# Optimization experiments

Measured on AMD Instinct MI355X. Metric: run time of the kernel, lower is better.

The kernel has to match this reference:

```python
import jax, jax.numpy as jnp
import numpy as np

DIM = 192
D_STATE = 16
D_CONV = 4
EXPAND = 2
D_INNER = EXPAND * DIM
DT_RANK = -(-DIM // 16)  # ceil(dim/16) = 12


def setup_inputs() -> dict:
    key = jax.random.key(0)
    ks = jax.random.split(key, 9)
    B, T, H, W, C = 2, 16, 28, 28, DIM
    x = jax.random.normal(ks[0], (B, T, H, W, C), dtype=jnp.float32)
    s = lambda k, shp, fan: jax.random.normal(k, shp, dtype=jnp.float32) / np.sqrt(fan)
    params = {
        "norm_w": jnp.ones((DIM,), jnp.float32),
        "in_proj_w": s(ks[1], (DIM, 2 * D_INNER), DIM),
        "conv_w": s(ks[2], (D_INNER, D_CONV), D_CONV),
        "conv_b": jnp.zeros((D_INNER,), jnp.float32),
        "x_proj_w": s(ks[3], (D_INNER, DT_RANK + 2 * D_STATE), D_INNER),
        "dt_proj_w": s(ks[4], (DT_RANK, D_INNER), DT_RANK),
        "dt_proj_b": jnp.full((D_INNER,), float(np.log(np.expm1(0.01))), jnp.float32),
        "A_log": jnp.log(jnp.broadcast_to(jnp.arange(1, D_STATE + 1, dtype=jnp.float32), (D_INNER, D_STATE))),
        "D": jnp.ones((D_INNER,), jnp.float32),
        "out_proj_w": s(ks[5], (D_INNER, DIM), D_INNER),
    }
    return {"x": x, **params}


def _mamba_block(xs, norm_w, in_proj_w, conv_w, conv_b, x_proj_w,
                 dt_proj_w, dt_proj_b, A_log, D, out_proj_w):
    # xs: (N, T, C). Pre-RMSNorm + Mamba + residual.
    nrm = jax.lax.rsqrt(jnp.mean(xs * xs, axis=-1, keepdims=True) + 1e-6)
    xn = xs * nrm * norm_w

    xz = xn @ in_proj_w                      # (N, T, 2*Din)
    u, z = jnp.split(xz, 2, axis=-1)         # each (N, T, Din)

    # causal depthwise conv over T
    uc = jnp.transpose(u, (0, 2, 1))         # (N, Din, T)
    uc = jax.lax.conv_general_dilated(
        uc, conv_w[:, None, :], window_strides=(1,),
        padding=[(D_CONV - 1, 0)], feature_group_count=D_INNER)
    uc = jax.nn.silu(uc + conv_b[None, :, None])
    uc = jnp.transpose(uc, (0, 2, 1))        # (N, T, Din)

    dbl = uc @ x_proj_w                      # (N, T, dt_rank + 2*S)
    dt, Bm, Cm = jnp.split(dbl, [DT_RANK, DT_RANK + D_STATE], axis=-1)
    dt = jax.nn.softplus(dt @ dt_proj_w + dt_proj_b)   # (N, T, Din)
    A = -jnp.exp(A_log)                      # (Din, S)

    def step(h, inp):
        dt_t, B_t, C_t, u_t = inp            # (N,Din),(N,S),(N,S),(N,Din)
        dA = jnp.exp(dt_t[..., None] * A)    # (N, Din, S)
        h = h * dA + (dt_t * u_t)[..., None] * B_t[:, None, :]
        y = jnp.einsum('nds,ns->nd', h, C_t)
        return h, y

    N = uc.shape[0]
    h0 = jnp.zeros((N, D_INNER, D_STATE), dt.dtype)
    sw = lambda a: jnp.swapaxes(a, 0, 1)     # time-major for scan
    _, ys = jax.lax.scan(step, h0, (sw(dt), sw(Bm), sw(Cm), sw(uc)))
    y = jnp.swapaxes(ys, 0, 1) + uc * D      # (N, T, Din)
    y = y * jax.nn.silu(z)
    return xs + y @ out_proj_w


def reference(x, norm_w, in_proj_w, conv_w, conv_b, x_proj_w,
              dt_proj_w, dt_proj_b, A_log, D, out_proj_w):
    B, T, H, W, C = x.shape
    xs = jnp.transpose(x, (0, 2, 3, 1, 4)).reshape(B * H * W, T, C)
    out = _mamba_block(xs, norm_w, in_proj_w, conv_w, conv_b, x_proj_w,
                       dt_proj_w, dt_proj_b, A_log, D, out_proj_w)
    return jnp.transpose(out.reshape(B, H, W, T, C), (0, 3, 1, 2, 4))
```

## Files before the change

kernel.cpp:

```cpp
#include <hip/hip_runtime.h>

#define NSEQ 1568
#define TDIM 16
#define CDIM 192
#define DIN  384
#define SDIM 16
#define RNK  12
#define XZW  768
#define DBLW 44
#define HW784 784

#define XNP  200
#define DINP 392
#define DBLP 48

#define NT_IN 48
#define KT_IN 6
#define NT_OUT 12
#define KT_OUT 12
#define NT_XP 3
#define KT_XP 12
#define GRP_IN  (NT_IN*KT_IN*64)
#define GRP_OUT (NT_OUT*KT_OUT*64)
#define GRP_XP  (NT_XP*KT_XP*64)
#define OFF_OUT (GRP_IN*8)
#define OFF_XP  (OFF_OUT + GRP_OUT*8)
#define WS_NEED ((size_t)(OFF_XP + GRP_XP*8) * 2)

typedef unsigned short u16;
typedef unsigned int   u32;
typedef __attribute__((ext_vector_type(8))) short short8;
typedef __attribute__((ext_vector_type(4))) float f32x4;

#define LOG2E 1.44269504f
#define LN2   0.69314718f

__device__ __forceinline__ float bf2f(u16 u) {
  union { u32 i; float f; } c; c.i = ((u32)u) << 16; return c.f;
}
__device__ __forceinline__ float asf(u32 i) {
  union { u32 i; float f; } c; c.i = i; return c.f;
}
__device__ __forceinline__ u16 f2bf(float f) {
  union { float f; u32 i; } c; c.f = f;
  u32 i = c.i;
  i += 0x7FFFu + ((i >> 16) & 1u);
  return (u16)(i >> 16);
}

__device__ __forceinline__ float ex2(float x) {
#if __has_builtin(__builtin_amdgcn_exp2f)
  return __builtin_amdgcn_exp2f(x);
#else
  return exp2f(x);
#endif
}
__device__ __forceinline__ float lg2(float x) {
#if __has_builtin(__builtin_amdgcn_logf)
  return __builtin_amdgcn_logf(x);
#else
  return log2f(x);
#endif
}
__device__ __forceinline__ float frcp(float x) {
#if __has_builtin(__builtin_amdgcn_rcpf)
  return __builtin_amdgcn_rcpf(x);
#else
  return 1.0f / x;
#endif
}
__device__ __forceinline__ float sigmoid_f(float s) {
  return frcp(1.0f + ex2(-LOG2E * s));
}
__device__ __forceinline__ float softplus_f(float a) {
  return fmaxf(a, 0.f) + LN2 * lg2(1.0f + ex2(-LOG2E * fabsf(a)));
}

template<bool B16>
__device__ __forceinline__ float ldg(const void* p, int i) {
  if (B16) return bf2f(((const u16*)p)[i]);
  return ((const float*)p)[i];
}
template<bool B16>
__device__ __forceinline__ void stg(void* p, int i, float v) {
  if (B16) ((u16*)p)[i] = f2bf(v);
  else     ((float*)p)[i] = v;
}

__device__ __forceinline__ bool probe_bf16(const void* x) {
  const u16* xu = (const u16*)x;
  int plaus = 0;
  #pragma unroll
  for (int k = 0; k < 32; ++k) {
    u16 v = xu[2*k];
    int e = (v >> 7) & 0xFF;
    plaus += ((e >= 100 && e <= 140) || v == 0) ? 1 : 0;
  }
  return plaus >= 16;
}

template<bool B16>
__device__ __forceinline__ void pack_body(const void* in_w, const void* out_w,
                                          const void* xp_w, u16* ws, int g) {
  if (g < GRP_IN) {
    int lane = g & 63, kt = (g >> 6) % KT_IN, nt = g / (64*KT_IN);
    int k0 = kt*32 + (lane >> 4)*8, n = nt*16 + (lane & 15);
    u16* dst = ws + g*8;
    #pragma unroll
    for (int j = 0; j < 8; ++j) dst[j] = f2bf(ldg<B16>(in_w, (k0+j)*XZW + n));
  } else if (g < GRP_IN + GRP_OUT) {
    int gg = g - GRP_IN;
    int lane = gg & 63, kt = (gg >> 6) % KT_OUT, nt = gg / (64*KT_OUT);
    int k0 = kt*32 + (lane >> 4)*8, n = nt*16 + (lane & 15);
    u16* dst = ws + OFF_OUT + gg*8;
    #pragma unroll
    for (int j = 0; j < 8; ++j) dst[j] = f2bf(ldg<B16>(out_w, (k0+j)*CDIM + n));
  } else if (g < GRP_IN + GRP_OUT + GRP_XP) {
    int gg = g - GRP_IN - GRP_OUT;
    int lane = gg & 63, kt = (gg >> 6) % KT_XP, nt = gg / (64*KT_XP);
    int k0 = kt*32 + (lane >> 4)*8, n = nt*16 + (lane & 15);
    u16* dst = ws + OFF_XP + gg*8;
    #pragma unroll
    for (int j = 0; j < 8; ++j)
      dst[j] = f2bf(n < DBLW ? ldg<B16>(xp_w, (k0+j)*DBLW + n) : 0.f);
  }
}

__global__ void pack_w(const void* __restrict__ x, const void* __restrict__ in_w,
                       const void* __restrict__ out_w, const void* __restrict__ xp_w,
                       u16* __restrict__ ws) {
  int g = blockIdx.x * blockDim.x + threadIdx.x;
  if (probe_bf16(x)) pack_body<true >(in_w, out_w, xp_w, ws, g);
  else               pack_body<false>(in_w, out_w, xp_w, ws, g);
}

struct Smem {
  u16   xn [TDIM*XNP];
  u16   u  [TDIM*DINP];
  u16   z  [TDIM*DINP];
  float dbl[TDIM*DBLP];
};

template<bool B16>
__device__ __forceinline__ void body(
    Smem& sm, const u16* __restrict__ ws,
    const void* __restrict__ x,        const void* __restrict__ norm_w,
    const void* __restrict__ conv_w,   const void* __restrict__ conv_b,
    const void* __restrict__ dt_proj_w,const void* __restrict__ dt_proj_b,
    const void* __restrict__ A_log,    const void* __restrict__ Dp,
    void* __restrict__ out)
{
  const int tid  = threadIdx.x;
  const int wid  = tid >> 6;
  const int lane = tid & 63;
  const int quad = lane >> 4;
  const int l16  = lane & 15;
  const int n  = blockIdx.x;
  const int b  = n / HW784;
  const int hw = n - b * HW784;

  {
    const int c0 = lane, c1 = lane + 64, c2 = lane + 128;
    float nw0 = ldg<B16>(norm_w, c0), nw1 = ldg<B16>(norm_w, c1), nw2 = ldg<B16>(norm_w, c2);
    for (int t = wid; t < TDIM; t += 6) {
      int base = ((b*TDIM + t)*HW784 + hw)*CDIM;
      float v0 = ldg<B16>(x, base + c0);
      float v1 = ldg<B16>(x, base + c1);
      float v2 = ldg<B16>(x, base + c2);
      float ss = v0*v0 + v1*v1 + v2*v2;
      #pragma unroll
      for (int off = 32; off > 0; off >>= 1) ss += __shfl_xor(ss, off, 64);
      float rs = rsqrtf(ss * (1.0f/CDIM) + 1e-6f);
      sm.xn[t*XNP + c0] = f2bf(v0 * rs * nw0);
      sm.xn[t*XNP + c1] = f2bf(v1 * rs * nw1);
      sm.xn[t*XNP + c2] = f2bf(v2 * rs * nw2);
    }
  }
  __syncthreads();

  {
    short8 afr[KT_IN];
    #pragma unroll
    for (int kt = 0; kt < KT_IN; ++kt)
      afr[kt] = *(const short8*)(sm.xn + l16*XNP + kt*32 + quad*8);
    #pragma unroll
    for (int g = 0; g < 2; ++g) {
      f32x4 acc[4];
      #pragma unroll
      for (int i = 0; i < 4; ++i) acc[i] = (f32x4)0.f;
      #pragma unroll
      for (int kt = 0; kt < KT_IN; ++kt) {
        #pragma unroll
        for (int i = 0; i < 4; ++i) {
          int ntg = wid*8 + g*4 + i;
          short8 bfr = *(const short8*)(ws + ((ntg*KT_IN + kt)*64 + lane)*8);
          acc[i] = __builtin_amdgcn_mfma_f32_16x16x32_bf16(afr[kt], bfr, acc[i], 0, 0, 0);
        }
      }
      #pragma unroll
      for (int i = 0; i < 4; ++i) {
        int ntg = wid*8 + g*4 + i;
        u16* dst = (ntg < 24) ? sm.u : sm.z;
        int col = ((ntg < 24) ? ntg*16 : (ntg-24)*16) + l16;
        #pragma unroll
        for (int r = 0; r < 4; ++r)
          dst[(quad*4 + r)*DINP + col] = f2bf(acc[i][r]);
      }
    }
  }
  __syncthreads();

  {
    const int d = tid;
    float uv[TDIM];
    #pragma unroll
    for (int t = 0; t < TDIM; ++t) uv[t] = bf2f(sm.u[t*DINP + d]);
    float w0 = ldg<B16>(conv_w, d*4+0), w1 = ldg<B16>(conv_w, d*4+1);
    float w2 = ldg<B16>(conv_w, d*4+2), w3 = ldg<B16>(conv_w, d*4+3);
    float bias = ldg<B16>(conv_b, d);
    #pragma unroll
    for (int t = 0; t < TDIM; ++t) {
      float s = bias + uv[t]*w3;
      if (t >= 1) s += uv[t-1]*w2;
      if (t >= 2) s += uv[t-2]*w1;
      if (t >= 3) s += uv[t-3]*w0;
      sm.u[t*DINP + d] = f2bf(s * sigmoid_f(s));
    }
  }

  float wd[RNK], A2[SDIM];
  float dt_bias = ldg<B16>(dt_proj_b, tid);
  #pragma unroll
  for (int r = 0; r < RNK; ++r) wd[r] = ldg<B16>(dt_proj_w, r*DIN + tid);
  #pragma unroll
  for (int s = 0; s < SDIM; ++s)
    A2[s] = -LOG2E * ex2(LOG2E * ldg<B16>(A_log, tid*SDIM + s));
  float Dv = ldg<B16>(Dp, tid);
  __syncthreads();

  if (wid < 3) {
    f32x4 acc = (f32x4)0.f;
    #pragma unroll
    for (int kt = 0; kt < KT_XP; ++kt) {
      short8 afr = *(const short8*)(sm.u + l16*DINP + kt*32 + quad*8);
      short8 bfr = *(const short8*)(ws + OFF_XP + ((wid*KT_XP + kt)*64 + lane)*8);
      acc = __builtin_amdgcn_mfma_f32_16x16x32_bf16(afr, bfr, acc, 0, 0, 0);
    }
    #pragma unroll
    for (int r = 0; r < 4; ++r)
      sm.dbl[(quad*4 + r)*DBLP + wid*16 + l16] = acc[r];
  }
  __syncthreads();

  {
    const int d = tid;
    float h[SDIM];
    #pragma unroll
    for (int s = 0; s < SDIM; ++s) h[s] = 0.f;
    for (int t = 0; t < TDIM; ++t) {
      float a = dt_bias;
      #pragma unroll
      for (int r = 0; r < RNK; ++r) a += sm.dbl[t*DBLP + r] * wd[r];
      float dtv = softplus_f(a);
      float uv  = bf2f(sm.u[t*DINP + d]);
      float du  = dtv * uv;
      float y = 0.f;
      #pragma unroll
      for (int s = 0; s < SDIM; ++s) {
        float dA = ex2(dtv * A2[s]);
        h[s] = h[s]*dA + du * sm.dbl[t*DBLP + 12 + s];
        y += h[s] * sm.dbl[t*DBLP + 28 + s];
      }
      y += uv * Dv;
      float zv = bf2f(sm.z[t*DINP + d]);
      sm.z[t*DINP + d] = f2bf(y * (zv * sigmoid_f(zv)));
    }
  }
  __syncthreads();

  {
    f32x4 acc[2];
    acc[0] = (f32x4)0.f; acc[1] = (f32x4)0.f;
    #pragma unroll
    for (int kt = 0; kt < KT_OUT; ++kt) {
      short8 afr = *(const short8*)(sm.z + l16*DINP + kt*32 + quad*8);
      #pragma unroll
      for (int i = 0; i < 2; ++i) {
        int ntg = wid*2 + i;
        short8 bfr = *(const short8*)(ws + OFF_OUT + ((ntg*KT_OUT + kt)*64 + lane)*8);
        acc[i] = __builtin_amdgcn_mfma_f32_16x16x32_bf16(afr, bfr, acc[i], 0, 0, 0);
      }
    }
    #pragma unroll
    for (int i = 0; i < 2; ++i) {
      int col = (wid*2 + i)*16 + l16;
      #pragma unroll
      for (int r = 0; r < 4; ++r) {
        int row = quad*4 + r;
        int gi = ((b*TDIM + row)*HW784 + hw)*CDIM + col;
        float o = ldg<B16>(x, gi) + acc[i][r];
        stg<B16>(out, gi, o);
      }
    }
  }
}

__launch_bounds__(384, 6)
__global__ void mamba_mfma(
    const u16* __restrict__ ws,
    const void* __restrict__ x,        const void* __restrict__ norm_w,
    const void* __restrict__ conv_w,   const void* __restrict__ conv_b,
    const void* __restrict__ dt_proj_w,const void* __restrict__ dt_proj_b,
    const void* __restrict__ A_log,    const void* __restrict__ Dp,
    void* __restrict__ out)
{
  __shared__ Smem sm;
  if (probe_bf16(x))
    body<true >(sm, ws, x, norm_w, conv_w, conv_b, dt_proj_w, dt_proj_b, A_log, Dp, out);
  else
    body<false>(sm, ws, x, norm_w, conv_w, conv_b, dt_proj_w, dt_proj_b, A_log, Dp, out);
}

struct SmemF {
  float dt [TDIM*DIN];
  float dbl[TDIM*DBLW];
  u16   xs [TDIM*CDIM];
  u16   xn [TDIM*CDIM];
  u16   u  [TDIM*DIN];
  u16   z  [TDIM*DIN];
};

template<bool B16>
__device__ __forceinline__ void body_fb(
    SmemF& sm,
    const void* __restrict__ x,        const void* __restrict__ norm_w,
    const void* __restrict__ in_proj_w,const void* __restrict__ conv_w,
    const void* __restrict__ conv_b,   const void* __restrict__ x_proj_w,
    const void* __restrict__ dt_proj_w,const void* __restrict__ dt_proj_b,
    const void* __restrict__ A_log,    const void* __restrict__ Dp,
    const void* __restrict__ out_proj_w, void* __restrict__ out)
{
  const int tid = threadIdx.x;
  const int n  = blockIdx.x;
  const int b  = n / HW784;
  const int hw = n - b * HW784;

  for (int i = tid; i < TDIM*CDIM; i += 384) {
    int t = i / CDIM, c = i - t * CDIM;
    sm.xs[i] = f2bf(ldg<B16>(x, ((b*TDIM + t)*HW784 + hw)*CDIM + c));
  }
  __syncthreads();
  {
    int wave = tid >> 6, lane = tid & 63;
    for (int t = wave; t < TDIM; t += 6) {
      float ss = 0.f;
      for (int c = lane; c < CDIM; c += 64) {
        float v = bf2f(sm.xs[t*CDIM + c]); ss += v*v;
      }
      #pragma unroll
      for (int off = 32; off > 0; off >>= 1) ss += __shfl_xor(ss, off, 64);
      float rs = rsqrtf(ss * (1.0f/CDIM) + 1e-6f);
      for (int c = lane; c < CDIM; c += 64)
        sm.xn[t*CDIM + c] = f2bf(bf2f(sm.xs[t*CDIM + c]) * rs * ldg<B16>(norm_w, c));
    }
  }
  __syncthreads();
  {
    float acc0[TDIM], acc1[TDIM];
    #pragma unroll
    for (int t = 0; t < TDIM; ++t) { acc0[t] = 0.f; acc1[t] = 0.f; }
    const int j0 = 2 * tid;
    for (int c = 0; c < CDIM; c += 2) {
      float wA0 = ldg<B16>(in_proj_w,  c   *XZW + j0);
      float wA1 = ldg<B16>(in_proj_w,  c   *XZW + j0 + 1);
      float wB0 = ldg<B16>(in_proj_w, (c+1)*XZW + j0);
      float wB1 = ldg<B16>(in_proj_w, (c+1)*XZW + j0 + 1);
      #pragma unroll
      for (int t = 0; t < TDIM; ++t) {
        u32 xv = *(const u32*)(sm.xn + t*CDIM + c);
        float x0 = asf(xv << 16), x1 = asf(xv & 0xFFFF0000u);
        acc0[t] += x0*wA0 + x1*wB0;
        acc1[t] += x0*wA1 + x1*wB1;
      }
    }
    if (tid < 192) {
      #pragma unroll
      for (int t = 0; t < TDIM; ++t) {
        sm.u[t*DIN + j0]   = f2bf(acc0[t]);
        sm.u[t*DIN + j0+1] = f2bf(acc1[t]);
      }
    } else {
      int z0 = j0 - 384;
      #pragma unroll
      for (int t = 0; t < TDIM; ++t) {
        sm.z[t*DIN + z0]   = f2bf(acc0[t]);
        sm.z[t*DIN + z0+1] = f2bf(acc1[t]);
      }
    }
  }
  __syncthreads();
  {
    const int d = tid;
    float uv[TDIM];
    #pragma unroll
    for (int t = 0; t < TDIM; ++t) uv[t] = bf2f(sm.u[t*DIN + d]);
    float w0 = ldg<B16>(conv_w, d*4+0), w1 = ldg<B16>(conv_w, d*4+1);
    float w2 = ldg<B16>(conv_w, d*4+2), w3 = ldg<B16>(conv_w, d*4+3);
    float bias = ldg<B16>(conv_b, d);
    #pragma unroll
    for (int t = 0; t < TDIM; ++t) {
      float s = bias + uv[t]*w3;
      if (t >= 1) s += uv[t-1]*w2;
      if (t >= 2) s += uv[t-2]*w1;
      if (t >= 3) s += uv[t-3]*w0;
      float sg = 1.0f / (1.0f + __expf(-s));
      sm.u[t*DIN + d] = f2bf(s * sg);
    }
  }
  __syncthreads();
  for (int o = tid; o < TDIM*DBLW; o += 384) {
    int t = o / DBLW, j = o - t*DBLW;
    float acc = 0.f;
    for (int d = 0; d < DIN; ++d)
      acc += bf2f(sm.u[t*DIN + d]) * ldg<B16>(x_proj_w, d*DBLW + j);
    sm.dbl[o] = acc;
  }
  __syncthreads();
  {
    const int d = tid;
    float wd[RNK];
    #pragma unroll
    for (int r = 0; r < RNK; ++r) wd[r] = ldg<B16>(dt_proj_w, r*DIN + d);
    float bias = ldg<B16>(dt_proj_b, d);
    #pragma unroll
    for (int t = 0; t < TDIM; ++t) {
      float a = bias;
      #pragma unroll
      for (int r = 0; r < RNK; ++r) a += sm.dbl[t*DBLW + r] * wd[r];
      sm.dt[t*DIN + d] = fmaxf(a, 0.f) + log1pf(__expf(-fabsf(a)));
    }
  }
  __syncthreads();
  {
    const int d = tid;
    float A[SDIM], h[SDIM];
    #pragma unroll
    for (int s = 0; s < SDIM; ++s) {
      A[s] = -__expf(ldg<B16>(A_log, d*SDIM + s));
      h[s] = 0.f;
    }
    float Dv = ldg<B16>(Dp, d);
    for (int t = 0; t < TDIM; ++t) {
      float dtv = sm.dt[t*DIN + d];
      float uv  = bf2f(sm.u[t*DIN + d]);
      float du  = dtv * uv;
      float y = 0.f;
      #pragma unroll
      for (int s = 0; s < SDIM; ++s) {
        float dA = __expf(dtv * A[s]);
        h[s] = h[s]*dA + du * sm.dbl[t*DBLW + 12 + s];
        y += h[s] * sm.dbl[t*DBLW + 28 + s];
      }
      y += uv * Dv;
      float zv = bf2f(sm.z[t*DIN + d]);
      float sg = 1.0f / (1.0f + __expf(-zv));
      sm.dt[t*DIN + d] = y * (zv * sg);
    }
  }
  __syncthreads();
  {
    const int tt = tid / CDIM;
    const int c  = tid - tt*CDIM;
    float acc[8];
    #pragma unroll
    for (int i = 0; i < 8; ++i) acc[i] = 0.f;
    for (int d = 0; d < DIN; ++d) {
      float w = ldg<B16>(out_proj_w, d*CDIM + c);
      #pragma unroll
      for (int i = 0; i < 8; ++i)
        acc[i] += sm.dt[(tt*8 + i)*DIN + d] * w;
    }
    #pragma unroll
    for (int i = 0; i < 8; ++i) {
      int t = tt*8 + i;
      float o = bf2f(sm.xs[t*CDIM + c]) + acc[i];
      stg<B16>(out, ((b*TDIM + t)*HW784 + hw)*CDIM + c, o);
    }
  }
}

__launch_bounds__(384)
__global__ void mamba_fallback(
    const void* __restrict__ x,        const void* __restrict__ norm_w,
    const void* __restrict__ in_proj_w,const void* __restrict__ conv_w,
    const void* __restrict__ conv_b,   const void* __restrict__ x_proj_w,
    const void* __restrict__ dt_proj_w,const void* __restrict__ dt_proj_b,
    const void* __restrict__ A_log,    const void* __restrict__ Dp,
    const void* __restrict__ out_proj_w, void* __restrict__ out)
{
  __shared__ SmemF sm;
  if (probe_bf16(x))
    body_fb<true >(sm, x, norm_w, in_proj_w, conv_w, conv_b, x_proj_w,
                   dt_proj_w, dt_proj_b, A_log, Dp, out_proj_w, out);
  else
    body_fb<false>(sm, x, norm_w, in_proj_w, conv_w, conv_b, x_proj_w,
                   dt_proj_w, dt_proj_b, A_log, Dp, out_proj_w, out);
}

extern "C" void kernel_launch(void* const* d_in, const int* in_sizes, int n_in,
                              void* d_out, int out_size, void* d_ws, size_t ws_size,
                              hipStream_t stream) {
  if (ws_size >= WS_NEED) {
    int packThreads = GRP_IN + GRP_OUT + GRP_XP;
    pack_w<<<(packThreads + 255) / 256, 256, 0, stream>>>(
        d_in[0], d_in[2], d_in[10], d_in[5], (u16*)d_ws);
    mamba_mfma<<<NSEQ, 384, 0, stream>>>(
        (const u16*)d_ws,
        d_in[0], d_in[1], d_in[3], d_in[4],
        d_in[6], d_in[7], d_in[8], d_in[9], d_out);
  } else {
    mamba_fallback<<<NSEQ, 384, 0, stream>>>(
        d_in[0], d_in[1], d_in[2], d_in[3], d_in[4], d_in[5],
        d_in[6], d_in[7], d_in[8], d_in[9], d_in[10], d_out);
  }
}
```

Baseline: 185.9 us.

## Use geometric A structure to replace per-state exps with powers in scan

Detects at runtime whether A_log encodes A[s]=(s+1)*A[0] per channel, and if so computes one exp2 per timestep and derives all 16 decay factors by repeated multiplication instead of 16 exp2 calls. A fallback path keeps the general per-state exp. It also repacks weights with one element per thread for coalesced reads, vectorizes dbl row reads from LDS as float4, streams the causal conv with rolling registers, and moves dbl to the front of shared memory for alignment. Products of powers can drift slightly from direct exps, and the check adds 16 exps per thread up front.

```diff
diff --git a/kernel.cpp b/kernel.cpp
--- a/kernel.cpp
+++ b/kernel.cpp
@@ -27,6 +27,11 @@
 #define OFF_XP  (OFF_OUT + GRP_OUT*8)
 #define WS_NEED ((size_t)(OFF_XP + GRP_XP*8) * 2)
 
+#define IN_EL  (CDIM*XZW)
+#define OUT_EL (DIN*CDIM)
+#define XP_EL  (GRP_XP*8)
+#define PACK_TOT (IN_EL + OUT_EL + XP_EL)
+
 typedef unsigned short u16;
 typedef unsigned int   u32;
 typedef __attribute__((ext_vector_type(8))) short short8;
@@ -37,9 +42,6 @@
 
 __device__ __forceinline__ float bf2f(u16 u) {
   union { u32 i; float f; } c; c.i = ((u32)u) << 16; return c.f;
-}
-__device__ __forceinline__ float asf(u32 i) {
-  union { u32 i; float f; } c; c.i = i; return c.f;
 }
 __device__ __forceinline__ u16 f2bf(float f) {
   union { float f; u32 i; } c; c.f = f;
@@ -101,44 +103,40 @@
 
 template<bool B16>
 __device__ __forceinline__ void pack_body(const void* in_w, const void* out_w,
-                                          const void* xp_w, u16* ws, int g) {
-  if (g < GRP_IN) {
-    int lane = g & 63, kt = (g >> 6) % KT_IN, nt = g / (64*KT_IN);
-    int k0 = kt*32 + (lane >> 4)*8, n = nt*16 + (lane & 15);
-    u16* dst = ws + g*8;
-    #pragma unroll
-    for (int j = 0; j < 8; ++j) dst[j] = f2bf(ldg<B16>(in_w, (k0+j)*XZW + n));
-  } else if (g < GRP_IN + GRP_OUT) {
-    int gg = g - GRP_IN;
-    int lane = gg & 63, kt = (gg >> 6) % KT_OUT, nt = gg / (64*KT_OUT);
-    int k0 = kt*32 + (lane >> 4)*8, n = nt*16 + (lane & 15);
-    u16* dst = ws + OFF_OUT + gg*8;
-    #pragma unroll
-    for (int j = 0; j < 8; ++j) dst[j] = f2bf(ldg<B16>(out_w, (k0+j)*CDIM + n));
-  } else if (g < GRP_IN + GRP_OUT + GRP_XP) {
-    int gg = g - GRP_IN - GRP_OUT;
+                                          const void* xp_w, u16* ws, int e) {
+  if (e < IN_EL) {
+    int k = e / XZW, n = e - k*XZW;
+    int nt = n >> 4, l16 = n & 15, kt = k >> 5, q8 = (k & 31) >> 3, j = k & 7;
+    int lane = q8*16 + l16;
+    ws[((nt*KT_IN + kt)*64 + lane)*8 + j] = f2bf(ldg<B16>(in_w, e));
+  } else if (e < IN_EL + OUT_EL) {
+    int ee = e - IN_EL;
+    int k = ee / CDIM, n = ee - k*CDIM;
+    int nt = n >> 4, l16 = n & 15, kt = k >> 5, q8 = (k & 31) >> 3, j = k & 7;
+    int lane = q8*16 + l16;
+    ws[OFF_OUT + ((nt*KT_OUT + kt)*64 + lane)*8 + j] = f2bf(ldg<B16>(out_w, ee));
+  } else if (e < PACK_TOT) {
+    int ee = e - IN_EL - OUT_EL;
+    int gg = ee >> 3, j = ee & 7;
     int lane = gg & 63, kt = (gg >> 6) % KT_XP, nt = gg / (64*KT_XP);
-    int k0 = kt*32 + (lane >> 4)*8, n = nt*16 + (lane & 15);
-    u16* dst = ws + OFF_XP + gg*8;
-    #pragma unroll
-    for (int j = 0; j < 8; ++j)
-      dst[j] = f2bf(n < DBLW ? ldg<B16>(xp_w, (k0+j)*DBLW + n) : 0.f);
+    int k = kt*32 + (lane >> 4)*8 + j, n = nt*16 + (lane & 15);
+    ws[OFF_XP + ee] = f2bf(n < DBLW ? ldg<B16>(xp_w, k*DBLW + n) : 0.f);
   }
 }
 
 __global__ void pack_w(const void* __restrict__ x, const void* __restrict__ in_w,
                        const void* __restrict__ out_w, const void* __restrict__ xp_w,
                        u16* __restrict__ ws) {
-  int g = blockIdx.x * blockDim.x + threadIdx.x;
-  if (probe_bf16(x)) pack_body<true >(in_w, out_w, xp_w, ws, g);
-  else               pack_body<false>(in_w, out_w, xp_w, ws, g);
+  int e = blockIdx.x * blockDim.x + threadIdx.x;
+  if (probe_bf16(x)) pack_body<true >(in_w, out_w, xp_w, ws, e);
+  else               pack_body<false>(in_w, out_w, xp_w, ws, e);
 }
 
 struct Smem {
+  float dbl[TDIM*DBLP];
   u16   xn [TDIM*XNP];
   u16   u  [TDIM*DINP];
   u16   z  [TDIM*DINP];
-  float dbl[TDIM*DBLP];
 };
 
 template<bool B16>
@@ -212,30 +210,35 @@
 
   {
     const int d = tid;
-    float uv[TDIM];
-    #pragma unroll
-    for (int t = 0; t < TDIM; ++t) uv[t] = bf2f(sm.u[t*DINP + d]);
     float w0 = ldg<B16>(conv_w, d*4+0), w1 = ldg<B16>(conv_w, d*4+1);
     float w2 = ldg<B16>(conv_w, d*4+2), w3 = ldg<B16>(conv_w, d*4+3);
     float bias = ldg<B16>(conv_b, d);
+    float um1 = 0.f, um2 = 0.f, um3 = 0.f;
     #pragma unroll
     for (int t = 0; t < TDIM; ++t) {
-      float s = bias + uv[t]*w3;
-      if (t >= 1) s += uv[t-1]*w2;
-      if (t >= 2) s += uv[t-2]*w1;
-      if (t >= 3) s += uv[t-3]*w0;
+      float cur = bf2f(sm.u[t*DINP + d]);
+      float s = bias + cur*w3 + um1*w2 + um2*w1 + um3*w0;
+      um3 = um2; um2 = um1; um1 = cur;
       sm.u[t*DINP + d] = f2bf(s * sigmoid_f(s));
     }
   }
 
-  float wd[RNK], A2[SDIM];
+  float wd[RNK];
   float dt_bias = ldg<B16>(dt_proj_b, tid);
   #pragma unroll
   for (int r = 0; r < RNK; ++r) wd[r] = ldg<B16>(dt_proj_w, r*DIN + tid);
-  #pragma unroll
-  for (int s = 0; s < SDIM; ++s)
-    A2[s] = -LOG2E * ex2(LOG2E * ldg<B16>(A_log, tid*SDIM + s));
   float Dv = ldg<B16>(Dp, tid);
+  float a2;
+  bool geo;
+  {
+    a2 = -LOG2E * ex2(LOG2E * ldg<B16>(A_log, tid*SDIM + 0));
+    geo = true;
+    #pragma unroll
+    for (int s = 1; s < SDIM; ++s) {
+      float as = -LOG2E * ex2(LOG2E * ldg<B16>(A_log, tid*SDIM + s));
+      geo = geo && (fabsf(as - (float)(s+1)*a2) <= 1e-4f * fabsf(as) + 1e-30f);
+    }
+  }
   __syncthreads();
 
   if (wid < 3) {
@@ -257,23 +260,75 @@
     float h[SDIM];
     #pragma unroll
     for (int s = 0; s < SDIM; ++s) h[s] = 0.f;
-    for (int t = 0; t < TDIM; ++t) {
-      float a = dt_bias;
-      #pragma unroll
-      for (int r = 0; r < RNK; ++r) a += sm.dbl[t*DBLP + r] * wd[r];
-      float dtv = softplus_f(a);
-      float uv  = bf2f(sm.u[t*DINP + d]);
-      float du  = dtv * uv;
-      float y = 0.f;
-      #pragma unroll
-      for (int s = 0; s < SDIM; ++s) {
-        float dA = ex2(dtv * A2[s]);
-        h[s] = h[s]*dA + du * sm.dbl[t*DBLP + 12 + s];
-        y += h[s] * sm.dbl[t*DBLP + 28 + s];
-      }
-      y += uv * Dv;
-      float zv = bf2f(sm.z[t*DINP + d]);
-      sm.z[t*DINP + d] = f2bf(y * (zv * sigmoid_f(zv)));
+    if (geo) {
+      for (int t = 0; t < TDIM; ++t) {
+        const float* row = sm.dbl + t*DBLP;
+        f32x4 d0 = *(const f32x4*)(row + 0);
+        f32x4 d1 = *(const f32x4*)(row + 4);
+        f32x4 d2 = *(const f32x4*)(row + 8);
+        float a = dt_bias
+          + d0[0]*wd[0] + d0[1]*wd[1] + d0[2]*wd[2]  + d0[3]*wd[3]
+          + d1[0]*wd[4] + d1[1]*wd[5] + d1[2]*wd[6]  + d1[3]*wd[7]
+          + d2[0]*wd[8] + d2[1]*wd[9] + d2[2]*wd[10] + d2[3]*wd[11];
+        float dtv = softplus_f(a);
+        float uv  = bf2f(sm.u[t*DINP + d]);
+        float du  = dtv * uv;
+        float q = ex2(dtv * a2);
+        float Pq[SDIM];
+        Pq[0] = q;        Pq[1] = q*q;       Pq[2] = Pq[1]*q;     Pq[3] = Pq[1]*Pq[1];
+        Pq[4] = Pq[3]*q;  Pq[5] = Pq[3]*Pq[1]; Pq[6] = Pq[3]*Pq[2]; Pq[7] = Pq[3]*Pq[3];
+        Pq[8] = Pq[7]*q;  Pq[9] = Pq[7]*Pq[1]; Pq[10]= Pq[7]*Pq[2]; Pq[11]= Pq[7]*Pq[3];
+        Pq[12]= Pq[7]*Pq[4]; Pq[13]= Pq[7]*Pq[5]; Pq[14]= Pq[7]*Pq[6]; Pq[15]= Pq[7]*Pq[7];
+        float y = 0.f;
+        #pragma unroll
+        for (int g = 0; g < 4; ++g) {
+          f32x4 Bv = *(const f32x4*)(row + 12 + 4*g);
+          f32x4 Cv = *(const f32x4*)(row + 28 + 4*g);
+          #pragma unroll
+          for (int j = 0; j < 4; ++j) {
+            int s = 4*g + j;
+            h[s] = h[s]*Pq[s] + du*Bv[j];
+            y += h[s]*Cv[j];
+          }
+        }
+        y += uv * Dv;
+        float zv = bf2f(sm.z[t*DINP + d]);
+        sm.z[t*DINP + d] = f2bf(y * (zv * sigmoid_f(zv)));
+      }
+    } else {
+      float A2[SDIM];
+      #pragma unroll
+      for (int s = 0; s < SDIM; ++s)
+        A2[s] = -LOG2E * ex2(LOG2E * ldg<B16>(A_log, d*SDIM + s));
+      for (int t = 0; t < TDIM; ++t) {
+        const float* row = sm.dbl + t*DBLP;
+        f32x4 d0 = *(const f32x4*)(row + 0);
+        f32x4 d1 = *(const f32x4*)(row + 4);
+        f32x4 d2 = *(const f32x4*)(row + 8);
+        float a = dt_bias
+          + d0[0]*wd[0] + d0[1]*wd[1] + d0[2]*wd[2]  + d0[3]*wd[3]
+          + d1[0]*wd[4] + d1[1]*wd[5] + d1[2]*wd[6]  + d1[3]*wd[7]
+          + d2[0]*wd[8] + d2[1]*wd[9] + d2[2]*wd[10] + d2[3]*wd[11];
+        float dtv = softplus_f(a);
+        float uv  = bf2f(sm.u[t*DINP + d]);
+        float du  = dtv * uv;
+        float y = 0.f;
+        #pragma unroll
+        for (int g = 0; g < 4; ++g) {
+          f32x4 Bv = *(const f32x4*)(row + 12 + 4*g);
+          f32x4 Cv = *(const f32x4*)(row + 28 + 4*g);
+          #pragma unroll
+          for (int j = 0; j < 4; ++j) {
+            int s = 4*g + j;
+            float dA = ex2(dtv * A2[s]);
+            h[s] = h[s]*dA + du*Bv[j];
+            y += h[s]*Cv[j];
+          }
+        }
+        y += uv * Dv;
+        float zv = bf2f(sm.z[t*DINP + d]);
+        sm.z[t*DINP + d] = f2bf(y * (zv * sigmoid_f(zv)));
+      }
     }
   }
   __syncthreads();
@@ -377,10 +432,11 @@
       float wB1 = ldg<B16>(in_proj_w, (c+1)*XZW + j0 + 1);
       #pragma unroll
       for (int t = 0; t < TDIM; ++t) {
+        union { u32 i; float f; } c0, c1;
         u32 xv = *(const u32*)(sm.xn + t*CDIM + c);
-        float x0 = asf(xv << 16), x1 = asf(xv & 0xFFFF0000u);
-        acc0[t] += x0*wA0 + x1*wB0;
-        acc1[t] += x0*wA1 + x1*wB1;
+        c0.i = xv << 16; c1.i = xv & 0xFFFF0000u;
+        acc0[t] += c0.f*wA0 + c1.f*wB0;
+        acc1[t] += c0.f*wA1 + c1.f*wB1;
       }
     }
     if (tid < 192) {
@@ -511,8 +567,7 @@
                               void* d_out, int out_size, void* d_ws, size_t ws_size,
                               hipStream_t stream) {
   if (ws_size >= WS_NEED) {
-    int packThreads = GRP_IN + GRP_OUT + GRP_XP;
-    pack_w<<<(packThreads + 255) / 256, 256, 0, stream>>>(
+    pack_w<<<(PACK_TOT + 255) / 256, 256, 0, stream>>>(
         d_in[0], d_in[2], d_in[10], d_in[5], (u16*)d_ws);
     mamba_mfma<<<NSEQ, 384, 0, stream>>>(
         (const u16*)d_ws,
```

After: 170.9 us. -8.0%, faster.
